# Optimization experiments

Measured on AMD Instinct MI355X. Metric: run time of the kernel, lower is better.

Reference implementation:

```python
import jax, jax.numpy as jnp
import numpy as np

N_EMBD = 1024
N_HEAD = 16
HEAD_DIM = N_EMBD // N_HEAD
MASK_FILL = -10.0  # module uses -10, not -inf


def setup_inputs() -> dict:
    key = jax.random.key(0)
    kx, kq, kk, kv, ko = jax.random.split(key, 5)
    B, T = 4, 2048
    s = 1.0 / np.sqrt(N_EMBD)
    return {
        "x": jax.random.normal(kx, (B, T, N_EMBD), dtype=jnp.float32),
        "wq": jax.random.normal(kq, (N_EMBD, N_EMBD), dtype=jnp.float32) * s,
        "wk": jax.random.normal(kk, (N_EMBD, N_EMBD), dtype=jnp.float32) * s,
        "wv": jax.random.normal(kv, (N_EMBD, N_EMBD), dtype=jnp.float32) * s,
        "wo": jax.random.normal(ko, (N_EMBD, N_EMBD), dtype=jnp.float32) * s,
    }


def reference(x, wq, wk, wv, wo):
    B, T, C = x.shape
    # nn.Linear applies x @ W.T; weights here stored as [out, in]
    q = (x @ wq.T).reshape(B, T, N_HEAD, HEAD_DIM).transpose(0, 2, 1, 3)
    k = (x @ wk.T).reshape(B, T, N_HEAD, HEAD_DIM).transpose(0, 2, 1, 3)
    v = (x @ wv.T).reshape(B, T, N_HEAD, HEAD_DIM).transpose(0, 2, 1, 3)
    scale = 1.0 / np.sqrt(HEAD_DIM)
    att = jnp.einsum("bhqd,bhkd->bhqk", q, k) * scale  # [B,H,T,T]
    causal = jnp.tril(jnp.ones((T, T), dtype=bool))
    att = jnp.where(causal[None, None, :, :], att, MASK_FILL)
    att = jax.nn.softmax(att, axis=-1)
    y = jnp.einsum("bhqk,bhkd->bhqd", att, v)
    y = y.transpose(0, 2, 1, 3).reshape(B, T, C)
    return y @ wo.T
```

## Files before the change

kernel.cpp:

```cpp
#include <hip/hip_runtime.h>

typedef __attribute__((ext_vector_type(8))) short bf16x8;
typedef __attribute__((ext_vector_type(4))) float f32x4;

#define T_SEQ 2048
#define EXPM10 4.5399929762484854e-05f

__device__ __forceinline__ unsigned short f2bf(float f) {
    unsigned int u = __builtin_bit_cast(unsigned int, f);
    u += 0x7fffu + ((u >> 16) & 1u);
    return (unsigned short)(u >> 16);
}
__device__ __forceinline__ float bf2f(unsigned short u) {
    return __builtin_bit_cast(float, (unsigned int)u << 16);
}

__device__ __forceinline__ void async16(void* lds, const void* g) {
    __builtin_amdgcn_global_load_lds(
        (__attribute__((address_space(1))) void*)g,
        (__attribute__((address_space(3))) void*)lds, 16, 0, 0);
}

__global__ __launch_bounds__(256) void cvt_bf16(const float* __restrict__ src,
                                                unsigned short* __restrict__ dst, int n4) {
    int i = blockIdx.x * 256 + threadIdx.x;
    if (i < n4) {
        float4 v = ((const float4*)src)[i];
        ushort4 r;
        r.x = f2bf(v.x); r.y = f2bf(v.y); r.z = f2bf(v.z); r.w = f2bf(v.w);
        ((ushort4*)dst)[i] = r;
    }
}

__global__ __launch_bounds__(256) void cvt_w(const float* __restrict__ wq,
                                             const float* __restrict__ wk,
                                             const float* __restrict__ wv,
                                             const float* __restrict__ wo,
                                             unsigned short* __restrict__ wqkv,
                                             unsigned short* __restrict__ wob) {
    int which = blockIdx.x >> 10;
    int i = (blockIdx.x & 1023) * 256 + threadIdx.x;
    const float* src = which == 0 ? wq : which == 1 ? wk : which == 2 ? wv : wo;
    unsigned short* dst = which < 3 ? wqkv + (size_t)which * 1048576 : wob;
    float4 v = ((const float4*)src)[i];
    ushort4 r;
    r.x = f2bf(v.x); r.y = f2bf(v.y); r.z = f2bf(v.z); r.w = f2bf(v.w);
    ((ushort4*)dst)[i] = r;
}

__global__ __launch_bounds__(256) void gemm_qkv(const unsigned short* __restrict__ A,
                                                const unsigned short* __restrict__ B,
                                                unsigned short* __restrict__ Qb,
                                                unsigned short* __restrict__ Kb,
                                                unsigned short* __restrict__ Vtb) {
    __shared__ unsigned short As[128 * 32];
    __shared__ unsigned short Bs[128 * 32];
    const int K = 1024;
    int m0 = blockIdx.y * 128, n0 = blockIdx.x * 128;
    int tid = threadIdx.x;
    int wave = tid >> 6, lane = tid & 63;
    int r = lane & 15, q = lane >> 4;
    int wr = wave >> 1, wc = wave & 1;

    f32x4 acc[4][4];
#pragma unroll
    for (int i = 0; i < 4; i++)
#pragma unroll
        for (int j = 0; j < 4; j++) acc[i][j] = (f32x4){0.f, 0.f, 0.f, 0.f};

    for (int k0 = 0; k0 < K; k0 += 32) {
#pragma unroll
        for (int i = 0; i < 2; i++) {
            int li = i * 256 + tid;
            int row = li >> 2, kk = (li & 3) << 3;
            async16(&As[i * 2048 + wave * 512], &A[(size_t)(m0 + row) * K + k0 + kk]);
            async16(&Bs[i * 2048 + wave * 512], &B[(size_t)(n0 + row) * K + k0 + kk]);
        }
        __syncthreads();
        bf16x8 af[4], bfr[4];
#pragma unroll
        for (int mi = 0; mi < 4; mi++)
            af[mi] = *(const bf16x8*)&As[(wr * 64 + mi * 16 + r) * 32 + q * 8];
#pragma unroll
        for (int ni = 0; ni < 4; ni++)
            bfr[ni] = *(const bf16x8*)&Bs[(wc * 64 + ni * 16 + r) * 32 + q * 8];
#pragma unroll
        for (int mi = 0; mi < 4; mi++)
#pragma unroll
            for (int ni = 0; ni < 4; ni++)
                acc[mi][ni] = __builtin_amdgcn_mfma_f32_16x16x32_bf16(
                    af[mi], bfr[ni], acc[mi][ni], 0, 0, 0);
        __syncthreads();
    }

#pragma unroll
    for (int mi = 0; mi < 4; mi++) {
#pragma unroll
        for (int ni = 0; ni < 4; ni++) {
#pragma unroll
            for (int rr = 0; rr < 4; rr++) {
                int gm = m0 + wr * 64 + mi * 16 + q * 4 + rr;
                int gn = n0 + wc * 64 + ni * 16 + r;
                float v = acc[mi][ni][rr];
                int b = gm >> 11, t = gm & 2047;
                int sel = gn >> 10, nn = gn & 1023;
                int h = nn >> 6, d = nn & 63;
                if (sel == 0)
                    Qb[((size_t)(b * 16 + h) * 2048 + t) * 64 + d] = f2bf(v);
                else if (sel == 1)
                    Kb[((size_t)(b * 16 + h) * 2048 + t) * 64 + d] = f2bf(v);
                else
                    Vtb[((size_t)(b * 16 + h) * 64 + d) * 2048 + t] = f2bf(v);
            }
        }
    }
}

__global__ __launch_bounds__(256) void gemm_out(const unsigned short* __restrict__ A,
                                                const unsigned short* __restrict__ B,
                                                float* __restrict__ out) {
    __shared__ unsigned short As[128 * 32];
    __shared__ unsigned short Bs[128 * 32];
    const int K = 1024;
    int m0 = blockIdx.y * 128, n0 = blockIdx.x * 128;
    int tid = threadIdx.x;
    int wave = tid >> 6, lane = tid & 63;
    int r = lane & 15, q = lane >> 4;
    int wr = wave >> 1, wc = wave & 1;

    f32x4 acc[4][4];
#pragma unroll
    for (int i = 0; i < 4; i++)
#pragma unroll
        for (int j = 0; j < 4; j++) acc[i][j] = (f32x4){0.f, 0.f, 0.f, 0.f};

    for (int k0 = 0; k0 < K; k0 += 32) {
#pragma unroll
        for (int i = 0; i < 2; i++) {
            int li = i * 256 + tid;
            int row = li >> 2, kk = (li & 3) << 3;
            async16(&As[i * 2048 + wave * 512], &A[(size_t)(m0 + row) * K + k0 + kk]);
            async16(&Bs[i * 2048 + wave * 512], &B[(size_t)(n0 + row) * K + k0 + kk]);
        }
        __syncthreads();
        bf16x8 af[4], bfr[4];
#pragma unroll
        for (int mi = 0; mi < 4; mi++)
            af[mi] = *(const bf16x8*)&As[(wr * 64 + mi * 16 + r) * 32 + q * 8];
#pragma unroll
        for (int ni = 0; ni < 4; ni++)
            bfr[ni] = *(const bf16x8*)&Bs[(wc * 64 + ni * 16 + r) * 32 + q * 8];
#pragma unroll
        for (int mi = 0; mi < 4; mi++)
#pragma unroll
            for (int ni = 0; ni < 4; ni++)
                acc[mi][ni] = __builtin_amdgcn_mfma_f32_16x16x32_bf16(
                    af[mi], bfr[ni], acc[mi][ni], 0, 0, 0);
        __syncthreads();
    }

#pragma unroll
    for (int mi = 0; mi < 4; mi++)
#pragma unroll
        for (int ni = 0; ni < 4; ni++)
#pragma unroll
            for (int rr = 0; rr < 4; rr++) {
                int gm = m0 + wr * 64 + mi * 16 + q * 4 + rr;
                int gn = n0 + wc * 64 + ni * 16 + r;
                out[(size_t)gm * 1024 + gn] = acc[mi][ni][rr];
            }
}

__global__ __launch_bounds__(256) void suffix_sv(const unsigned short* __restrict__ Vt,
                                                 float* __restrict__ SV) {
    __shared__ float bsum[32][64];
    int bh = blockIdx.x;
    int d = threadIdx.x & 63, c = threadIdx.x >> 6;
    const unsigned short* base = Vt + ((size_t)bh * 64 + d) * T_SEQ;
#pragma unroll
    for (int jj = 0; jj < 8; jj++) {
        int j = c * 8 + jj;
        float s = 0.f;
#pragma unroll
        for (int t8 = 0; t8 < 8; t8++) {
            bf16x8 v = *(const bf16x8*)(base + j * 64 + t8 * 8);
#pragma unroll
            for (int e = 0; e < 8; e++) s += bf2f((unsigned short)v[e]);
        }
        bsum[j][d] = s;
    }
    __syncthreads();
    if (threadIdx.x < 64) {
        float run = 0.f;
        for (int j = 31; j >= 0; j--) {
            run += bsum[j][d];
            SV[((size_t)bh * 32 + j) * 64 + d] = run;
        }
    }
}

#define KST 72
#define VST 72
#define PST 72
__global__ __launch_bounds__(256) void attn(const unsigned short* __restrict__ Q,
                                            const unsigned short* __restrict__ Kg,
                                            const unsigned short* __restrict__ Vt,
                                            const float* __restrict__ SV,
                                            unsigned short* __restrict__ Y) {
    __shared__ unsigned short Ks[64 * KST];
    __shared__ unsigned short Vs[64 * VST];
    __shared__ unsigned short Ps[4][16 * PST];
    int bh = blockIdx.y;
    int qi = 31 - blockIdx.x;
    int q0 = qi * 64;
    int tid = threadIdx.x, wave = tid >> 6, lane = tid & 63;
    int r = lane & 15, qd = lane >> 4;
    int query = q0 + wave * 16 + r;

    const unsigned short* qptr = Q + ((size_t)bh * T_SEQ + query) * 64 + qd * 8;
    bf16x8 qf0 = *(const bf16x8*)qptr;
    bf16x8 qf1 = *(const bf16x8*)(qptr + 32);

    float l_lane = 0.0f;
    f32x4 o[4];
#pragma unroll
    for (int n = 0; n < 4; n++) o[n] = (f32x4){0.f, 0.f, 0.f, 0.f};

    int srow = tid >> 2, scol = (tid & 3) * 16;
    const unsigned short* kg = Kg + ((size_t)bh * T_SEQ + srow) * 64 + scol;
    const unsigned short* vg = Vt + ((size_t)bh * 64 + srow) * T_SEQ + scol;
    const float scale = 0.125f;

    bf16x8 pk0 = *(const bf16x8*)(kg);
    bf16x8 pk1 = *(const bf16x8*)(kg + 8);
    bf16x8 pv0 = *(const bf16x8*)(vg);
    bf16x8 pv1 = *(const bf16x8*)(vg + 8);

    int iters = qi + 1;
    for (int it = 0; it < iters; ++it) {
        __syncthreads();
        *(bf16x8*)&Ks[srow * KST + scol]     = pk0;
        *(bf16x8*)&Ks[srow * KST + scol + 8] = pk1;
        *(bf16x8*)&Vs[srow * VST + scol]     = pv0;
        *(bf16x8*)&Vs[srow * VST + scol + 8] = pv1;
        __syncthreads();
        if (it + 1 < iters) {
            size_t kn = (size_t)(it + 1) * 64;
            pk0 = *(const bf16x8*)(kg + kn * 64);
            pk1 = *(const bf16x8*)(kg + kn * 64 + 8);
            pv0 = *(const bf16x8*)(vg + kn);
            pv1 = *(const bf16x8*)(vg + kn + 8);
        }

        int k0 = it * 64;
        f32x4 st[4];
#pragma unroll
        for (int t = 0; t < 4; t++) {
            bf16x8 kf0 = *(const bf16x8*)&Ks[(t * 16 + r) * KST + qd * 8];
            bf16x8 kf1 = *(const bf16x8*)&Ks[(t * 16 + r) * KST + 32 + qd * 8];
            st[t] = (f32x4){0.f, 0.f, 0.f, 0.f};
            st[t] = __builtin_amdgcn_mfma_f32_16x16x32_bf16(kf0, qf0, st[t], 0, 0, 0);
            st[t] = __builtin_amdgcn_mfma_f32_16x16x32_bf16(kf1, qf1, st[t], 0, 0, 0);
        }

        float p[4][4], sum = 0.f;
        bool anymask = (k0 + 63 > q0 + wave * 16);
        if (anymask) {
#pragma unroll
            for (int t = 0; t < 4; t++)
#pragma unroll
                for (int e = 0; e < 4; e++) {
                    int kgidx = k0 + t * 16 + qd * 4 + e;
                    float pe = __expf(st[t][e] * scale);
                    p[t][e] = (kgidx <= query) ? pe : EXPM10;
                    sum += p[t][e];
                }
        } else {
#pragma unroll
            for (int t = 0; t < 4; t++)
#pragma unroll
                for (int e = 0; e < 4; e++) {
                    p[t][e] = __expf(st[t][e] * scale);
                    sum += p[t][e];
                }
        }
        l_lane += sum;

#pragma unroll
        for (int t = 0; t < 4; t++) {
            ushort4 pk;
            pk.x = f2bf(p[t][0]); pk.y = f2bf(p[t][1]);
            pk.z = f2bf(p[t][2]); pk.w = f2bf(p[t][3]);
            *(ushort4*)&Ps[wave][r * PST + t * 16 + qd * 4] = pk;
        }
        __builtin_amdgcn_sched_barrier(0);

        bf16x8 pf0 = *(const bf16x8*)&Ps[wave][r * PST + qd * 8];
        bf16x8 pf1 = *(const bf16x8*)&Ps[wave][r * PST + 32 + qd * 8];
#pragma unroll
        for (int n = 0; n < 4; n++) {
            bf16x8 vf0 = *(const bf16x8*)&Vs[(n * 16 + r) * VST + qd * 8];
            bf16x8 vf1 = *(const bf16x8*)&Vs[(n * 16 + r) * VST + 32 + qd * 8];
            o[n] = __builtin_amdgcn_mfma_f32_16x16x32_bf16(vf0, pf0, o[n], 0, 0, 0);
            o[n] = __builtin_amdgcn_mfma_f32_16x16x32_bf16(vf1, pf1, o[n], 0, 0, 0);
        }
    }

    float l_i = l_lane;
    l_i += __shfl_xor(l_i, 16);
    l_i += __shfl_xor(l_i, 32);

    float pm = 0.f, tail_l = 0.f;
    float sv[4][4];
#pragma unroll
    for (int n = 0; n < 4; n++)
#pragma unroll
        for (int e = 0; e < 4; e++) sv[n][e] = 0.f;
    if (qi < 31) {
        pm = EXPM10;
        tail_l = (float)(T_SEQ - 64 * (qi + 1)) * pm;
        const float* svp = SV + ((size_t)bh * 32 + qi + 1) * 64;
#pragma unroll
        for (int n = 0; n < 4; n++) {
            float4 f = *(const float4*)(svp + n * 16 + qd * 4);
            sv[n][0] = f.x; sv[n][1] = f.y; sv[n][2] = f.z; sv[n][3] = f.w;
        }
    }
    float inv = 1.0f / (l_i + tail_l);
    int b = bh >> 4, h = bh & 15;
#pragma unroll
    for (int n = 0; n < 4; n++) {
        ushort4 yk;
        yk.x = f2bf((o[n][0] + pm * sv[n][0]) * inv);
        yk.y = f2bf((o[n][1] + pm * sv[n][1]) * inv);
        yk.z = f2bf((o[n][2] + pm * sv[n][2]) * inv);
        yk.w = f2bf((o[n][3] + pm * sv[n][3]) * inv);
        *(ushort4*)&Y[(((size_t)b * T_SEQ + query) * 16 + h) * 64 + n * 16 + qd * 4] = yk;
    }
}

extern "C" void kernel_launch(void* const* d_in, const int* in_sizes, int n_in,
                              void* d_out, int out_size, void* d_ws, size_t ws_size,
                              hipStream_t stream) {
    const float* x  = (const float*)d_in[0];
    const float* wq = (const float*)d_in[1];
    const float* wk = (const float*)d_in[2];
    const float* wv = (const float*)d_in[3];
    const float* wo = (const float*)d_in[4];

    char* ws = (char*)d_ws;
    const size_t MB = 1u << 20;
    unsigned short* xb   = (unsigned short*)(ws);
    unsigned short* Qb   = (unsigned short*)(ws + 16 * MB);
    unsigned short* Kb   = (unsigned short*)(ws + 32 * MB);
    unsigned short* Vtb  = (unsigned short*)(ws + 48 * MB);
    unsigned short* wqkv = (unsigned short*)(ws + 64 * MB);
    unsigned short* wob  = (unsigned short*)(ws + 70 * MB);
    unsigned short* Yb   = xb;
    float* SVf = (float*)d_out;

    cvt_bf16<<<8192, 256, 0, stream>>>(x, xb, 2097152);
    cvt_w<<<4096, 256, 0, stream>>>(wq, wk, wv, wo, wqkv, wob);

    gemm_qkv<<<dim3(24, 64), 256, 0, stream>>>(xb, wqkv, Qb, Kb, Vtb);

    suffix_sv<<<64, 256, 0, stream>>>(Vtb, SVf);

    attn<<<dim3(32, 64), 256, 0, stream>>>(Qb, Kb, Vtb, SVf, Yb);

    gemm_out<<<dim3(8, 64), 256, 0, stream>>>(Yb, wob, (float*)d_out);
}
```

Before: 349.6 us.

## Pair causal query tiles per attention block and double K-step in GEMMs

New measurement: 310.3 us. 1.13x faster.

```diff
diff --git a/kernel.cpp b/kernel.cpp
--- a/kernel.cpp
+++ b/kernel.cpp
@@ -53,8 +53,8 @@
                                                 unsigned short* __restrict__ Qb,
                                                 unsigned short* __restrict__ Kb,
                                                 unsigned short* __restrict__ Vtb) {
-    __shared__ unsigned short As[128 * 32];
-    __shared__ unsigned short Bs[128 * 32];
+    __shared__ unsigned short As[2][4096];
+    __shared__ unsigned short Bs[2][4096];
     const int K = 1024;
     int m0 = blockIdx.y * 128, n0 = blockIdx.x * 128;
     int tid = threadIdx.x;
@@ -68,28 +68,33 @@
 #pragma unroll
         for (int j = 0; j < 4; j++) acc[i][j] = (f32x4){0.f, 0.f, 0.f, 0.f};
 
-    for (int k0 = 0; k0 < K; k0 += 32) {
-#pragma unroll
-        for (int i = 0; i < 2; i++) {
-            int li = i * 256 + tid;
-            int row = li >> 2, kk = (li & 3) << 3;
-            async16(&As[i * 2048 + wave * 512], &A[(size_t)(m0 + row) * K + k0 + kk]);
-            async16(&Bs[i * 2048 + wave * 512], &B[(size_t)(n0 + row) * K + k0 + kk]);
-        }
+    for (int k0 = 0; k0 < K; k0 += 64) {
+#pragma unroll
+        for (int s = 0; s < 2; s++)
+#pragma unroll
+            for (int i = 0; i < 2; i++) {
+                int li = i * 256 + tid;
+                int rw = li >> 2, kc = (li & 3) << 3;
+                async16(&As[s][i * 2048 + wave * 512], &A[(size_t)(m0 + rw) * K + k0 + s * 32 + kc]);
+                async16(&Bs[s][i * 2048 + wave * 512], &B[(size_t)(n0 + rw) * K + k0 + s * 32 + kc]);
+            }
         __syncthreads();
-        bf16x8 af[4], bfr[4];
-#pragma unroll
-        for (int mi = 0; mi < 4; mi++)
-            af[mi] = *(const bf16x8*)&As[(wr * 64 + mi * 16 + r) * 32 + q * 8];
-#pragma unroll
-        for (int ni = 0; ni < 4; ni++)
-            bfr[ni] = *(const bf16x8*)&Bs[(wc * 64 + ni * 16 + r) * 32 + q * 8];
-#pragma unroll
-        for (int mi = 0; mi < 4; mi++)
+#pragma unroll
+        for (int s = 0; s < 2; s++) {
+            bf16x8 af[4], bfr[4];
+#pragma unroll
+            for (int mi = 0; mi < 4; mi++)
+                af[mi] = *(const bf16x8*)&As[s][(wr * 64 + mi * 16 + r) * 32 + q * 8];
 #pragma unroll
             for (int ni = 0; ni < 4; ni++)
-                acc[mi][ni] = __builtin_amdgcn_mfma_f32_16x16x32_bf16(
-                    af[mi], bfr[ni], acc[mi][ni], 0, 0, 0);
+                bfr[ni] = *(const bf16x8*)&Bs[s][(wc * 64 + ni * 16 + r) * 32 + q * 8];
+#pragma unroll
+            for (int mi = 0; mi < 4; mi++)
+#pragma unroll
+                for (int ni = 0; ni < 4; ni++)
+                    acc[mi][ni] = __builtin_amdgcn_mfma_f32_16x16x32_bf16(
+                        af[mi], bfr[ni], acc[mi][ni], 0, 0, 0);
+        }
         __syncthreads();
     }
 
@@ -119,8 +124,8 @@
 __global__ __launch_bounds__(256) void gemm_out(const unsigned short* __restrict__ A,
                                                 const unsigned short* __restrict__ B,
                                                 float* __restrict__ out) {
-    __shared__ unsigned short As[128 * 32];
-    __shared__ unsigned short Bs[128 * 32];
+    __shared__ unsigned short As[2][4096];
+    __shared__ unsigned short Bs[2][4096];
     const int K = 1024;
     int m0 = blockIdx.y * 128, n0 = blockIdx.x * 128;
     int tid = threadIdx.x;
@@ -134,28 +139,33 @@
 #pragma unroll
         for (int j = 0; j < 4; j++) acc[i][j] = (f32x4){0.f, 0.f, 0.f, 0.f};
 
-    for (int k0 = 0; k0 < K; k0 += 32) {
-#pragma unroll
-        for (int i = 0; i < 2; i++) {
-            int li = i * 256 + tid;
-            int row = li >> 2, kk = (li & 3) << 3;
-            async16(&As[i * 2048 + wave * 512], &A[(size_t)(m0 + row) * K + k0 + kk]);
-            async16(&Bs[i * 2048 + wave * 512], &B[(size_t)(n0 + row) * K + k0 + kk]);
-        }
+    for (int k0 = 0; k0 < K; k0 += 64) {
+#pragma unroll
+        for (int s = 0; s < 2; s++)
+#pragma unroll
+            for (int i = 0; i < 2; i++) {
+                int li = i * 256 + tid;
+                int rw = li >> 2, kc = (li & 3) << 3;
+                async16(&As[s][i * 2048 + wave * 512], &A[(size_t)(m0 + rw) * K + k0 + s * 32 + kc]);
+                async16(&Bs[s][i * 2048 + wave * 512], &B[(size_t)(n0 + rw) * K + k0 + s * 32 + kc]);
+            }
         __syncthreads();
-        bf16x8 af[4], bfr[4];
-#pragma unroll
-        for (int mi = 0; mi < 4; mi++)
-            af[mi] = *(const bf16x8*)&As[(wr * 64 + mi * 16 + r) * 32 + q * 8];
-#pragma unroll
-        for (int ni = 0; ni < 4; ni++)
-            bfr[ni] = *(const bf16x8*)&Bs[(wc * 64 + ni * 16 + r) * 32 + q * 8];
-#pragma unroll
-        for (int mi = 0; mi < 4; mi++)
+#pragma unroll
+        for (int s = 0; s < 2; s++) {
+            bf16x8 af[4], bfr[4];
+#pragma unroll
+            for (int mi = 0; mi < 4; mi++)
+                af[mi] = *(const bf16x8*)&As[s][(wr * 64 + mi * 16 + r) * 32 + q * 8];
 #pragma unroll
             for (int ni = 0; ni < 4; ni++)
-                acc[mi][ni] = __builtin_amdgcn_mfma_f32_16x16x32_bf16(
-                    af[mi], bfr[ni], acc[mi][ni], 0, 0, 0);
+                bfr[ni] = *(const bf16x8*)&Bs[s][(wc * 64 + ni * 16 + r) * 32 + q * 8];
+#pragma unroll
+            for (int mi = 0; mi < 4; mi++)
+#pragma unroll
+                for (int ni = 0; ni < 4; ni++)
+                    acc[mi][ni] = __builtin_amdgcn_mfma_f32_16x16x32_bf16(
+                        af[mi], bfr[ni], acc[mi][ni], 0, 0, 0);
+        }
         __syncthreads();
     }
 
@@ -211,131 +221,136 @@
     __shared__ unsigned short Vs[64 * VST];
     __shared__ unsigned short Ps[4][16 * PST];
     int bh = blockIdx.y;
-    int qi = 31 - blockIdx.x;
-    int q0 = qi * 64;
     int tid = threadIdx.x, wave = tid >> 6, lane = tid & 63;
     int r = lane & 15, qd = lane >> 4;
-    int query = q0 + wave * 16 + r;
-
-    const unsigned short* qptr = Q + ((size_t)bh * T_SEQ + query) * 64 + qd * 8;
-    bf16x8 qf0 = *(const bf16x8*)qptr;
-    bf16x8 qf1 = *(const bf16x8*)(qptr + 32);
-
-    float l_lane = 0.0f;
-    f32x4 o[4];
-#pragma unroll
-    for (int n = 0; n < 4; n++) o[n] = (f32x4){0.f, 0.f, 0.f, 0.f};
+    int b = bh >> 4, h = bh & 15;
 
     int srow = tid >> 2, scol = (tid & 3) * 16;
     const unsigned short* kg = Kg + ((size_t)bh * T_SEQ + srow) * 64 + scol;
     const unsigned short* vg = Vt + ((size_t)bh * 64 + srow) * T_SEQ + scol;
     const float scale = 0.125f;
 
-    bf16x8 pk0 = *(const bf16x8*)(kg);
-    bf16x8 pk1 = *(const bf16x8*)(kg + 8);
-    bf16x8 pv0 = *(const bf16x8*)(vg);
-    bf16x8 pv1 = *(const bf16x8*)(vg + 8);
-
-    int iters = qi + 1;
-    for (int it = 0; it < iters; ++it) {
-        __syncthreads();
-        *(bf16x8*)&Ks[srow * KST + scol]     = pk0;
-        *(bf16x8*)&Ks[srow * KST + scol + 8] = pk1;
-        *(bf16x8*)&Vs[srow * VST + scol]     = pv0;
-        *(bf16x8*)&Vs[srow * VST + scol + 8] = pv1;
-        __syncthreads();
-        if (it + 1 < iters) {
-            size_t kn = (size_t)(it + 1) * 64;
-            pk0 = *(const bf16x8*)(kg + kn * 64);
-            pk1 = *(const bf16x8*)(kg + kn * 64 + 8);
-            pv0 = *(const bf16x8*)(vg + kn);
-            pv1 = *(const bf16x8*)(vg + kn + 8);
-        }
-
-        int k0 = it * 64;
-        f32x4 st[4];
-#pragma unroll
-        for (int t = 0; t < 4; t++) {
-            bf16x8 kf0 = *(const bf16x8*)&Ks[(t * 16 + r) * KST + qd * 8];
-            bf16x8 kf1 = *(const bf16x8*)&Ks[(t * 16 + r) * KST + 32 + qd * 8];
-            st[t] = (f32x4){0.f, 0.f, 0.f, 0.f};
-            st[t] = __builtin_amdgcn_mfma_f32_16x16x32_bf16(kf0, qf0, st[t], 0, 0, 0);
-            st[t] = __builtin_amdgcn_mfma_f32_16x16x32_bf16(kf1, qf1, st[t], 0, 0, 0);
-        }
-
-        float p[4][4], sum = 0.f;
-        bool anymask = (k0 + 63 > q0 + wave * 16);
-        if (anymask) {
-#pragma unroll
-            for (int t = 0; t < 4; t++)
-#pragma unroll
-                for (int e = 0; e < 4; e++) {
-                    int kgidx = k0 + t * 16 + qd * 4 + e;
-                    float pe = __expf(st[t][e] * scale);
-                    p[t][e] = (kgidx <= query) ? pe : EXPM10;
-                    sum += p[t][e];
-                }
-        } else {
-#pragma unroll
-            for (int t = 0; t < 4; t++)
-#pragma unroll
-                for (int e = 0; e < 4; e++) {
-                    p[t][e] = __expf(st[t][e] * scale);
-                    sum += p[t][e];
-                }
-        }
-        l_lane += sum;
-
-#pragma unroll
-        for (int t = 0; t < 4; t++) {
-            ushort4 pk;
-            pk.x = f2bf(p[t][0]); pk.y = f2bf(p[t][1]);
-            pk.z = f2bf(p[t][2]); pk.w = f2bf(p[t][3]);
-            *(ushort4*)&Ps[wave][r * PST + t * 16 + qd * 4] = pk;
-        }
-        __builtin_amdgcn_sched_barrier(0);
-
-        bf16x8 pf0 = *(const bf16x8*)&Ps[wave][r * PST + qd * 8];
-        bf16x8 pf1 = *(const bf16x8*)&Ps[wave][r * PST + 32 + qd * 8];
+#pragma unroll
+    for (int phase = 0; phase < 2; phase++) {
+        int qi = phase == 0 ? 16 + (int)blockIdx.x : 15 - (int)blockIdx.x;
+        int q0 = qi * 64;
+        int query = q0 + wave * 16 + r;
+
+        const unsigned short* qptr = Q + ((size_t)bh * T_SEQ + query) * 64 + qd * 8;
+        bf16x8 qf0 = *(const bf16x8*)qptr;
+        bf16x8 qf1 = *(const bf16x8*)(qptr + 32);
+
+        float l_lane = 0.0f;
+        f32x4 o[4];
+#pragma unroll
+        for (int n = 0; n < 4; n++) o[n] = (f32x4){0.f, 0.f, 0.f, 0.f};
+
+        bf16x8 pk0 = *(const bf16x8*)(kg);
+        bf16x8 pk1 = *(const bf16x8*)(kg + 8);
+        bf16x8 pv0 = *(const bf16x8*)(vg);
+        bf16x8 pv1 = *(const bf16x8*)(vg + 8);
+
+        int iters = qi + 1;
+        for (int it = 0; it < iters; ++it) {
+            __syncthreads();
+            *(bf16x8*)&Ks[srow * KST + scol]     = pk0;
+            *(bf16x8*)&Ks[srow * KST + scol + 8] = pk1;
+            *(bf16x8*)&Vs[srow * VST + scol]     = pv0;
+            *(bf16x8*)&Vs[srow * VST + scol + 8] = pv1;
+            __syncthreads();
+            if (it + 1 < iters) {
+                size_t kn = (size_t)(it + 1) * 64;
+                pk0 = *(const bf16x8*)(kg + kn * 64);
+                pk1 = *(const bf16x8*)(kg + kn * 64 + 8);
+                pv0 = *(const bf16x8*)(vg + kn);
+                pv1 = *(const bf16x8*)(vg + kn + 8);
+            }
+
+            int k0 = it * 64;
+            f32x4 st[4];
+#pragma unroll
+            for (int t = 0; t < 4; t++) {
+                bf16x8 kf0 = *(const bf16x8*)&Ks[(t * 16 + r) * KST + qd * 8];
+                bf16x8 kf1 = *(const bf16x8*)&Ks[(t * 16 + r) * KST + 32 + qd * 8];
+                st[t] = (f32x4){0.f, 0.f, 0.f, 0.f};
+                st[t] = __builtin_amdgcn_mfma_f32_16x16x32_bf16(kf0, qf0, st[t], 0, 0, 0);
+                st[t] = __builtin_amdgcn_mfma_f32_16x16x32_bf16(kf1, qf1, st[t], 0, 0, 0);
+            }
+
+            float p[4][4], sum = 0.f;
+            bool anymask = (k0 + 63 > q0 + wave * 16);
+            if (anymask) {
+#pragma unroll
+                for (int t = 0; t < 4; t++)
+#pragma unroll
+                    for (int e = 0; e < 4; e++) {
+                        int kgidx = k0 + t * 16 + qd * 4 + e;
+                        float pe = __expf(st[t][e] * scale);
+                        p[t][e] = (kgidx <= query) ? pe : EXPM10;
+                        sum += p[t][e];
+                    }
+            } else {
+#pragma unroll
+                for (int t = 0; t < 4; t++)
+#pragma unroll
+                    for (int e = 0; e < 4; e++) {
+                        p[t][e] = __expf(st[t][e] * scale);
+                        sum += p[t][e];
+                    }
+            }
+            l_lane += sum;
+
+#pragma unroll
+            for (int t = 0; t < 4; t++) {
+                ushort4 pk;
+                pk.x = f2bf(p[t][0]); pk.y = f2bf(p[t][1]);
+                pk.z = f2bf(p[t][2]); pk.w = f2bf(p[t][3]);
+                *(ushort4*)&Ps[wave][r * PST + t * 16 + qd * 4] = pk;
+            }
+            __builtin_amdgcn_sched_barrier(0);
+
+            bf16x8 pf0 = *(const bf16x8*)&Ps[wave][r * PST + qd * 8];
+            bf16x8 pf1 = *(const bf16x8*)&Ps[wave][r * PST + 32 + qd * 8];
+#pragma unroll
+            for (int n = 0; n < 4; n++) {
+                bf16x8 vf0 = *(const bf16x8*)&Vs[(n * 16 + r) * VST + qd * 8];
+                bf16x8 vf1 = *(const bf16x8*)&Vs[(n * 16 + r) * VST + 32 + qd * 8];
+                o[n] = __builtin_amdgcn_mfma_f32_16x16x32_bf16(vf0, pf0, o[n], 0, 0, 0);
+                o[n] = __builtin_amdgcn_mfma_f32_16x16x32_bf16(vf1, pf1, o[n], 0, 0, 0);
+            }
+        }
+
+        float l_i = l_lane;
+        l_i += __shfl_xor(l_i, 16);
+        l_i += __shfl_xor(l_i, 32);
+
+        int j = qi + 1;
+        float pm = 0.f, tail_l = 0.f;
+        float sv[4][4];
+#pragma unroll
+        for (int n = 0; n < 4; n++)
+#pragma unroll
+            for (int e = 0; e < 4; e++) sv[n][e] = 0.f;
+        if (j < 32) {
+            pm = EXPM10;
+            tail_l = (float)(T_SEQ - 64 * j) * pm;
+            const float* svp = SV + ((size_t)bh * 32 + j) * 64;
+#pragma unroll
+            for (int n = 0; n < 4; n++) {
+                float4 f = *(const float4*)(svp + n * 16 + qd * 4);
+                sv[n][0] = f.x; sv[n][1] = f.y; sv[n][2] = f.z; sv[n][3] = f.w;
+            }
+        }
+        float inv = 1.0f / (l_i + tail_l);
 #pragma unroll
         for (int n = 0; n < 4; n++) {
-            bf16x8 vf0 = *(const bf16x8*)&Vs[(n * 16 + r) * VST + qd * 8];
-            bf16x8 vf1 = *(const bf16x8*)&Vs[(n * 16 + r) * VST + 32 + qd * 8];
-            o[n] = __builtin_amdgcn_mfma_f32_16x16x32_bf16(vf0, pf0, o[n], 0, 0, 0);
-            o[n] = __builtin_amdgcn_mfma_f32_16x16x32_bf16(vf1, pf1, o[n], 0, 0, 0);
-        }
-    }
-
-    float l_i = l_lane;
-    l_i += __shfl_xor(l_i, 16);
-    l_i += __shfl_xor(l_i, 32);
-
-    float pm = 0.f, tail_l = 0.f;
-    float sv[4][4];
-#pragma unroll
-    for (int n = 0; n < 4; n++)
-#pragma unroll
-        for (int e = 0; e < 4; e++) sv[n][e] = 0.f;
-    if (qi < 31) {
-        pm = EXPM10;
-        tail_l = (float)(T_SEQ - 64 * (qi + 1)) * pm;
-        const float* svp = SV + ((size_t)bh * 32 + qi + 1) * 64;
-#pragma unroll
-        for (int n = 0; n < 4; n++) {
-            float4 f = *(const float4*)(svp + n * 16 + qd * 4);
-            sv[n][0] = f.x; sv[n][1] = f.y; sv[n][2] = f.z; sv[n][3] = f.w;
-        }
-    }
-    float inv = 1.0f / (l_i + tail_l);
-    int b = bh >> 4, h = bh & 15;
-#pragma unroll
-    for (int n = 0; n < 4; n++) {
-        ushort4 yk;
-        yk.x = f2bf((o[n][0] + pm * sv[n][0]) * inv);
-        yk.y = f2bf((o[n][1] + pm * sv[n][1]) * inv);
-        yk.z = f2bf((o[n][2] + pm * sv[n][2]) * inv);
-        yk.w = f2bf((o[n][3] + pm * sv[n][3]) * inv);
-        *(ushort4*)&Y[(((size_t)b * T_SEQ + query) * 16 + h) * 64 + n * 16 + qd * 4] = yk;
+            ushort4 yk;
+            yk.x = f2bf((o[n][0] + pm * sv[n][0]) * inv);
+            yk.y = f2bf((o[n][1] + pm * sv[n][1]) * inv);
+            yk.z = f2bf((o[n][2] + pm * sv[n][2]) * inv);
+            yk.w = f2bf((o[n][3] + pm * sv[n][3]) * inv);
+            *(ushort4*)&Y[(((size_t)b * T_SEQ + query) * 16 + h) * 64 + n * 16 + qd * 4] = yk;
+        }
     }
 }
 
@@ -366,7 +381,7 @@
 
     suffix_sv<<<64, 256, 0, stream>>>(Vtb, SVf);
 
-    attn<<<dim3(32, 64), 256, 0, stream>>>(Qb, Kb, Vtb, SVf, Yb);
+    attn<<<dim3(16, 64), 256, 0, stream>>>(Qb, Kb, Vtb, SVf, Yb);
 
     gemm_out<<<dim3(8, 64), 256, 0, stream>>>(Yb, wob, (float*)d_out);
 }
```
